# Optimization experiments

Measured on AMD Instinct MI355X. Metric: run time of the kernel, lower is better.

The kernel has to match this reference:

```python
import jax, jax.numpy as jnp
import numpy as np
import math

INPUT_DIM = 1024
SCALE = 1.0


def hadamard_transform(u):
    """Unnormalized Walsh-Hadamard transform H_n @ u along the last axis.
    Faithful to the torch recursive cat/slice implementation (Sylvester order).
    u: (..., n) with n a power of 2."""
    n = u.shape[-1]
    m = int(np.log2(n))
    assert n == 1 << m, 'n must be a power of 2'
    x = u[..., None]  # (..., n, 1)
    for _ in range(m):
        even = x[..., ::2, :]
        odd = x[..., 1::2, :]
        x = jnp.concatenate([even + odd, even - odd], axis=-1)
    return x.squeeze(-2)  # (..., n)


def setup_inputs() -> dict:
    key = jax.random.key(0)
    kx, kb, kg, ks, kp = jax.random.split(key, 5)
    d = INPUT_DIM
    x = jax.random.normal(kx, (2, 2048, 16, d), dtype=jnp.float32)
    # B is a random sign vector, G is gaussian, S is chi-distributed / ||G||.
    B = jnp.where(jax.random.uniform(kb, (d,)) < 0.5, -1.0, 1.0).astype(jnp.float32)
    G = jax.random.normal(kg, (d,), dtype=jnp.float32)
    S = jnp.abs(jax.random.normal(ks, (d,), dtype=jnp.float32)) * math.sqrt(d) / jnp.linalg.norm(G)
    P = jax.random.permutation(kp, d)  # permutation indices, int
    return {'x': x, 'B': B, 'G': G, 'S': S, 'P': P}


def reference(x, B, G, S, P):
    x_shape = x.shape
    d = x_shape[-1]
    x_run = x.reshape(-1, d)                     # (R, d)
    Bx = x_run * B                               # elementwise sign flip
    HBx = hadamard_transform(Bx)                 # first butterfly
    PHBx = HBx[:, P]                             # permutation gather
    GPHBx = PHBx * G                             # gaussian scale
    HGPHBx = hadamard_transform(GPHBx)           # second butterfly
    SHGPHBx = HGPHBx * S                         # chi scale
    Vx = (1.0 / (SCALE * math.sqrt(d))) * SHGPHBx
    return Vx.reshape(x_shape)
```

## Files before the change

### kernel.cpp

```cpp
#include <hip/hip_runtime.h>


constexpr int D = 1024;
constexpr int THREADS = 256;
constexpr int WAVES_PER_BLOCK = 4;
constexpr int ROWS_PER_WAVE = 8;
constexpr int ROWS_PER_BLOCK = WAVES_PER_BLOCK * ROWS_PER_WAVE;

#if defined(__has_builtin)
#if __has_builtin(__builtin_amdgcn_permlane16_swap) && __has_builtin(__builtin_amdgcn_permlane32_swap)
#define HAS_PLSWAP 1
#endif
#endif

template <int CTRL>
__device__ __forceinline__ float dppmov(float x) {
    return __int_as_float(
        __builtin_amdgcn_update_dpp(0, __float_as_int(x), CTRL, 0xF, 0xF, false));
}

__device__ __forceinline__ void fwht1024(float v[16], float sg1, float sg2,
                                         float sg4, float sg8, float sg16,
                                         float sg32) {
    #pragma unroll
    for (int h = 1; h <= 8; h <<= 1) {
        #pragma unroll
        for (int j = 0; j < 16; ++j) {
            if ((j & h) == 0) {
                float a = v[j], c = v[j ^ h];
                v[j]     = a + c;
                v[j ^ h] = a - c;
            }
        }
    }
    #pragma unroll
    for (int j = 0; j < 16; ++j) {
        float p = dppmov<0xB1>(v[j]);
        v[j] = fmaf(sg1, v[j], p);
    }
    #pragma unroll
    for (int j = 0; j < 16; ++j) {
        float p = dppmov<0x4E>(v[j]);
        v[j] = fmaf(sg2, v[j], p);
    }
    #pragma unroll
    for (int j = 0; j < 16; ++j) {
        float p = dppmov<0x141>(dppmov<0x1B>(v[j]));
        v[j] = fmaf(sg4, v[j], p);
    }
    #pragma unroll
    for (int j = 0; j < 16; ++j) {
        float p = dppmov<0x128>(v[j]);
        v[j] = fmaf(sg8, v[j], p);
    }
#ifdef HAS_PLSWAP
    #pragma unroll
    for (int j = 0; j < 16; ++j) {
        auto r = __builtin_amdgcn_permlane16_swap(__float_as_uint(v[j]),
                                                  __float_as_uint(v[j]), false, false);
        v[j] = fmaf(sg16, __uint_as_float(r[1]), __uint_as_float(r[0]));
    }
    #pragma unroll
    for (int j = 0; j < 16; ++j) {
        auto r = __builtin_amdgcn_permlane32_swap(__float_as_uint(v[j]),
                                                  __float_as_uint(v[j]), false, false);
        v[j] = fmaf(sg32, __uint_as_float(r[1]), __uint_as_float(r[0]));
    }
#else
    #pragma unroll
    for (int j = 0; j < 16; ++j) {
        float p = __shfl_xor(v[j], 16, 64);
        v[j] = fmaf(sg16, v[j], p);
    }
    #pragma unroll
    for (int j = 0; j < 16; ++j) {
        float p = __shfl_xor(v[j], 32, 64);
        v[j] = fmaf(sg32, v[j], p);
    }
#endif
}

__global__ __launch_bounds__(THREADS) void fastfood_kernel(
    const float* __restrict__ x,
    const float* __restrict__ Bv,
    const float* __restrict__ Gv,
    const float* __restrict__ Sv,
    const int*   __restrict__ Pv,
    float* __restrict__ out)
{
    __shared__ float lds[WAVES_PER_BLOCK * D];

    const int lane  = threadIdx.x & 63;
    const int wave  = threadIdx.x >> 6;
    float* slice    = lds + wave * D;
    const int ebase = lane << 4;

    const float sg1  = (lane & 1)  ? -1.0f : 1.0f;
    const float sg2  = (lane & 2)  ? -1.0f : 1.0f;
    const float sg4  = (lane & 4)  ? -1.0f : 1.0f;
    const float sg8  = (lane & 8)  ? -1.0f : 1.0f;
    const float sg16 = (lane & 16) ? -1.0f : 1.0f;
    const float sg32 = (lane & 32) ? -1.0f : 1.0f;

    float b[16], g[16], s[16];
    int   p[16];
    #pragma unroll
    for (int q = 0; q < 4; ++q) {
        float4 tb = reinterpret_cast<const float4*>(Bv + ebase)[q];
        float4 tg = reinterpret_cast<const float4*>(Gv + ebase)[q];
        float4 ts = reinterpret_cast<const float4*>(Sv + ebase)[q];
        int4   tp = reinterpret_cast<const int4 *>(Pv + ebase)[q];
        const float inv = 1.0f / 32.0f;
        b[4*q+0]=tb.x; b[4*q+1]=tb.y; b[4*q+2]=tb.z; b[4*q+3]=tb.w;
        g[4*q+0]=tg.x; g[4*q+1]=tg.y; g[4*q+2]=tg.z; g[4*q+3]=tg.w;
        s[4*q+0]=ts.x*inv; s[4*q+1]=ts.y*inv; s[4*q+2]=ts.z*inv; s[4*q+3]=ts.w*inv;
        p[4*q+0]=tp.x; p[4*q+1]=tp.y; p[4*q+2]=tp.z; p[4*q+3]=tp.w;
    }

    for (int i = 0; i < ROWS_PER_WAVE; ++i) {
        const int row = blockIdx.x * ROWS_PER_BLOCK + i * WAVES_PER_BLOCK + wave;
        const float* xr = x + (size_t)row * D;

        float v[16];
        #pragma unroll
        for (int q = 0; q < 4; ++q) {
            float4 t = reinterpret_cast<const float4*>(xr + ebase)[q];
            v[4*q+0] = t.x * b[4*q+0];
            v[4*q+1] = t.y * b[4*q+1];
            v[4*q+2] = t.z * b[4*q+2];
            v[4*q+3] = t.w * b[4*q+3];
        }

        fwht1024(v, sg1, sg2, sg4, sg8, sg16, sg32);

        #pragma unroll
        for (int q = 0; q < 4; ++q) {
            reinterpret_cast<float4*>(slice + ebase)[q] =
                make_float4(v[4*q+0], v[4*q+1], v[4*q+2], v[4*q+3]);
        }
        #pragma unroll
        for (int j = 0; j < 16; ++j)
            v[j] = slice[p[j]] * g[j];

        fwht1024(v, sg1, sg2, sg4, sg8, sg16, sg32);

        float* outr = out + (size_t)row * D;
        #pragma unroll
        for (int q = 0; q < 4; ++q) {
            float4 t;
            t.x = v[4*q+0] * s[4*q+0];
            t.y = v[4*q+1] * s[4*q+1];
            t.z = v[4*q+2] * s[4*q+2];
            t.w = v[4*q+3] * s[4*q+3];
            reinterpret_cast<float4*>(outr + ebase)[q] = t;
        }
    }
}

extern "C" void kernel_launch(void* const* d_in, const int* in_sizes, int n_in,
                              void* d_out, int out_size, void* d_ws, size_t ws_size,
                              hipStream_t stream) {
    const float* x  = (const float*)d_in[0];
    const float* Bv = (const float*)d_in[1];
    const float* Gv = (const float*)d_in[2];
    const float* Sv = (const float*)d_in[3];
    const int*   Pv = (const int*)d_in[4];
    float* out = (float*)d_out;

    const int nrows  = in_sizes[0] / D;
    const int blocks = nrows / ROWS_PER_BLOCK;
    fastfood_kernel<<<blocks, THREADS, 0, stream>>>(x, Bv, Gv, Sv, Pv, out);
}
```

Baseline: 464.4 us.

## Prefetch next row with nontemporal loads and pack permutation offsets

Measured after the change: 761.1 us. 1.64x slower.

```diff
diff --git a/kernel.cpp b/kernel.cpp
--- a/kernel.cpp
+++ b/kernel.cpp
@@ -6,6 +6,8 @@
 constexpr int WAVES_PER_BLOCK = 4;
 constexpr int ROWS_PER_WAVE = 8;
 constexpr int ROWS_PER_BLOCK = WAVES_PER_BLOCK * ROWS_PER_WAVE;
+
+typedef float fx4 __attribute__((ext_vector_type(4)));
 
 #if defined(__has_builtin)
 #if __has_builtin(__builtin_amdgcn_permlane16_swap) && __has_builtin(__builtin_amdgcn_permlane32_swap)
@@ -80,6 +82,14 @@
 #endif
 }
 
+__device__ __forceinline__ void load_row_nt(float t[16], const float* __restrict__ xr) {
+    #pragma unroll
+    for (int q = 0; q < 4; ++q) {
+        fx4 f = __builtin_nontemporal_load(reinterpret_cast<const fx4*>(xr) + q);
+        t[4*q+0] = f.x; t[4*q+1] = f.y; t[4*q+2] = f.z; t[4*q+3] = f.w;
+    }
+}
+
 __global__ __launch_bounds__(THREADS) void fastfood_kernel(
     const float* __restrict__ x,
     const float* __restrict__ Bv,
@@ -93,6 +103,7 @@
     const int lane  = threadIdx.x & 63;
     const int wave  = threadIdx.x >> 6;
     float* slice    = lds + wave * D;
+    const char* sliceb = reinterpret_cast<const char*>(slice);
     const int ebase = lane << 4;
 
     const float sg1  = (lane & 1)  ? -1.0f : 1.0f;
@@ -103,7 +114,7 @@
     const float sg32 = (lane & 32) ? -1.0f : 1.0f;
 
     float b[16], g[16], s[16];
-    int   p[16];
+    unsigned po[8];
     #pragma unroll
     for (int q = 0; q < 4; ++q) {
         float4 tb = reinterpret_cast<const float4*>(Bv + ebase)[q];
@@ -114,21 +125,27 @@
         b[4*q+0]=tb.x; b[4*q+1]=tb.y; b[4*q+2]=tb.z; b[4*q+3]=tb.w;
         g[4*q+0]=tg.x; g[4*q+1]=tg.y; g[4*q+2]=tg.z; g[4*q+3]=tg.w;
         s[4*q+0]=ts.x*inv; s[4*q+1]=ts.y*inv; s[4*q+2]=ts.z*inv; s[4*q+3]=ts.w*inv;
-        p[4*q+0]=tp.x; p[4*q+1]=tp.y; p[4*q+2]=tp.z; p[4*q+3]=tp.w;
+        po[2*q+0] = (unsigned)(tp.x << 2) | ((unsigned)(tp.y << 2) << 16);
+        po[2*q+1] = (unsigned)(tp.z << 2) | ((unsigned)(tp.w << 2) << 16);
     }
 
+    const int row0 = blockIdx.x * ROWS_PER_BLOCK + wave;
+    const size_t rowstep = (size_t)WAVES_PER_BLOCK * D;
+    const float* xr   = x   + (size_t)row0 * D + ebase;
+    float*       outr = out + (size_t)row0 * D + ebase;
+
+    float t[16];
+    load_row_nt(t, xr);
+
     for (int i = 0; i < ROWS_PER_WAVE; ++i) {
-        const int row = blockIdx.x * ROWS_PER_BLOCK + i * WAVES_PER_BLOCK + wave;
-        const float* xr = x + (size_t)row * D;
-
         float v[16];
         #pragma unroll
-        for (int q = 0; q < 4; ++q) {
-            float4 t = reinterpret_cast<const float4*>(xr + ebase)[q];
-            v[4*q+0] = t.x * b[4*q+0];
-            v[4*q+1] = t.y * b[4*q+1];
-            v[4*q+2] = t.z * b[4*q+2];
-            v[4*q+3] = t.w * b[4*q+3];
+        for (int j = 0; j < 16; ++j)
+            v[j] = t[j] * b[j];
+
+        if (i + 1 < ROWS_PER_WAVE) {
+            xr += rowstep;
+            load_row_nt(t, xr);
         }
 
         fwht1024(v, sg1, sg2, sg4, sg8, sg16, sg32);
@@ -139,21 +156,26 @@
                 make_float4(v[4*q+0], v[4*q+1], v[4*q+2], v[4*q+3]);
         }
         #pragma unroll
-        for (int j = 0; j < 16; ++j)
-            v[j] = slice[p[j]] * g[j];
+        for (int k = 0; k < 8; ++k) {
+            const unsigned pk = po[k];
+            const float a0 = *reinterpret_cast<const float*>(sliceb + (pk & 0xFFFFu));
+            const float a1 = *reinterpret_cast<const float*>(sliceb + (pk >> 16));
+            v[2*k+0] = a0 * g[2*k+0];
+            v[2*k+1] = a1 * g[2*k+1];
+        }
 
         fwht1024(v, sg1, sg2, sg4, sg8, sg16, sg32);
 
-        float* outr = out + (size_t)row * D;
         #pragma unroll
         for (int q = 0; q < 4; ++q) {
-            float4 t;
-            t.x = v[4*q+0] * s[4*q+0];
-            t.y = v[4*q+1] * s[4*q+1];
-            t.z = v[4*q+2] * s[4*q+2];
-            t.w = v[4*q+3] * s[4*q+3];
-            reinterpret_cast<float4*>(outr + ebase)[q] = t;
+            fx4 o;
+            o.x = v[4*q+0] * s[4*q+0];
+            o.y = v[4*q+1] * s[4*q+1];
+            o.z = v[4*q+2] * s[4*q+2];
+            o.w = v[4*q+3] * s[4*q+3];
+            __builtin_nontemporal_store(o, reinterpret_cast<fx4*>(outr) + q);
         }
+        outr += rowstep;
     }
 }
 
```
